# Optimization experiments

Hardware: AMD Instinct MI355X
Metric: run time of the kernel (lower is better)

Reference implementation:

```python
import jax, jax.numpy as jnp
import numpy as np

B, N, E, H = 4, 4096, 1024, 16
D = E // H


def setup_inputs() -> dict:
    key = jax.random.key(0)
    ks = jax.random.split(key, 8)
    s = 1.0 / np.sqrt(E)
    x = jax.random.normal(ks[0], (B, N, E), dtype=jnp.float32)
    # binary multiplicative sparsity pattern over the head-head score matrix
    sparsity_pattern = jax.random.randint(ks[1], (H, H), 0, 2).astype(jnp.float32)
    Wq = jax.random.normal(ks[2], (E, E), dtype=jnp.float32) * s
    bq = jax.random.normal(ks[3], (E,), dtype=jnp.float32) * s
    Wk = jax.random.normal(ks[4], (E, E), dtype=jnp.float32) * s
    bk = jax.random.normal(ks[5], (E,), dtype=jnp.float32) * s
    Wv = jax.random.normal(ks[6], (E, E), dtype=jnp.float32) * s
    bv = jax.random.normal(ks[7], (E,), dtype=jnp.float32) * s
    return {"x": x, "sparsity_pattern": sparsity_pattern,
            "Wq": Wq, "bq": bq, "Wk": Wk, "bk": bk, "Wv": Wv, "bv": bv}


def reference(x, sparsity_pattern, Wq, bq, Wk, bk, Wv, bv):
    b, n, e = x.shape
    # torch Linear: y = x @ W.T + b
    q = (x @ Wq.T + bq).reshape(b, n, H, D)
    k = (x @ Wk.T + bk).reshape(b, n, H, D)
    v = (x @ Wv.T + bv).reshape(b, n, H, D)
    # torch.matmul over last two dims of [B,N,H,D]: scores are [B,N,H,H]
    scores = jnp.einsum('bnhd,bngd->bnhg', q, k) * sparsity_pattern
    attn = jax.nn.softmax(scores, axis=-1)
    out = jnp.einsum('bnhg,bngd->bnhd', attn, v).reshape(b, n, e)
    return out
```

## Files before the change

### kernel.cpp

```cpp
#include <hip/hip_runtime.h>
#include <hip/hip_bf16.h>

#define M_   16384
#define K_   1024
#define NQKV 3072

typedef _Float16 f16x4 __attribute__((ext_vector_type(4)));
typedef _Float16 f16x8 __attribute__((ext_vector_type(8)));
typedef float    f32x4 __attribute__((ext_vector_type(4)));

__global__ __launch_bounds__(256) void cvt_f32_f16(const float* __restrict__ in,
                                                   _Float16* __restrict__ o, int n4) {
  int i = blockIdx.x * blockDim.x + threadIdx.x;
  const int stride = gridDim.x * blockDim.x;
  for (; i < n4; i += stride) {
    float4 v = ((const float4*)in)[i];
    f16x4 h; h[0] = (_Float16)v.x; h[1] = (_Float16)v.y;
    h[2] = (_Float16)v.z; h[3] = (_Float16)v.w;
    *(f16x4*)&o[(size_t)i * 4] = h;
  }
}

__global__ __launch_bounds__(256) void gemm_qkv(
    const _Float16* __restrict__ xh, const _Float16* __restrict__ wh,
    const float* __restrict__ bq, const float* __restrict__ bk,
    const float* __restrict__ bv, _Float16* __restrict__ qkv)
{
  __shared__ __align__(16) _Float16 As[128 * 64];
  __shared__ __align__(16) _Float16 Bs[128 * 64];

  const int tid  = threadIdx.x;
  const int ln   = tid & 63;
  const int w    = tid >> 6;
  const int wm   = w >> 1, wn = w & 1;
  const int lcol = ln & 15, quad = ln >> 4;

  const int m0 = blockIdx.y * 128;
  const int n0 = blockIdx.x * 128;

  f32x4 acc[4][4];
#pragma unroll
  for (int i = 0; i < 4; i++)
#pragma unroll
    for (int j = 0; j < 4; j++) acc[i][j] = f32x4{0.f, 0.f, 0.f, 0.f};

  for (int k0 = 0; k0 < K_; k0 += 64) {
#pragma unroll
    for (int i = 0; i < 4; ++i) {
      const int cb  = w * 256 + i * 64;
      const int c   = cb + ln;
      const int row = c >> 3, cc = c & 7;
      __builtin_amdgcn_global_load_lds(
          (const __attribute__((address_space(1))) void*)(xh + (size_t)(m0 + row) * K_ + k0 + cc * 8),
          (__attribute__((address_space(3))) void*)(As + (size_t)cb * 8), 16, 0, 0);
      __builtin_amdgcn_global_load_lds(
          (const __attribute__((address_space(1))) void*)(wh + (size_t)(n0 + row) * K_ + k0 + cc * 8),
          (__attribute__((address_space(3))) void*)(Bs + (size_t)cb * 8), 16, 0, 0);
    }
    __syncthreads();

#pragma unroll
    for (int kk = 0; kk < 64; kk += 32) {
      f16x8 a[4], b[4];
#pragma unroll
      for (int mi = 0; mi < 4; mi++)
        a[mi] = *(const f16x8*)&As[(wm * 64 + mi * 16 + lcol) * 64 + kk + quad * 8];
#pragma unroll
      for (int ni = 0; ni < 4; ni++)
        b[ni] = *(const f16x8*)&Bs[(wn * 64 + ni * 16 + lcol) * 64 + kk + quad * 8];
#pragma unroll
      for (int mi = 0; mi < 4; mi++)
#pragma unroll
        for (int ni = 0; ni < 4; ni++)
          acc[mi][ni] = __builtin_amdgcn_mfma_f32_16x16x32_f16(a[mi], b[ni], acc[mi][ni], 0, 0, 0);
    }
    __syncthreads();
  }

#pragma unroll
  for (int ni = 0; ni < 4; ni++) {
    const int col = n0 + wn * 64 + ni * 16 + lcol;
    const int seg = col >> 10, cs = col & 1023;
    const float bi = ((seg == 0) ? bq : (seg == 1) ? bk : bv)[cs];
#pragma unroll
    for (int mi = 0; mi < 4; mi++) {
      const int r0 = m0 + wm * 64 + mi * 16 + quad * 4;
#pragma unroll
      for (int r = 0; r < 4; r++)
        qkv[(size_t)(r0 + r) * 3072 + col] = (_Float16)(acc[mi][ni][r] + bi);
    }
  }
}

__global__ __launch_bounds__(256) void attn_kernel(
    const _Float16* __restrict__ qkv,
    const float* __restrict__ pat,
    float* __restrict__ out)
{
  __shared__ float pat_s[256];
  __shared__ __align__(16) _Float16 Ps[4][16 * 24];
  __shared__ __align__(16) _Float16 Vt[4][64 * 24];

  const int tid  = threadIdx.x;
  const int ln   = tid & 63;
  const int wv   = tid >> 6;
  const int lcol = ln & 15, quad = ln >> 4;
  const int t    = blockIdx.x * 4 + wv;

  pat_s[tid] = pat[tid];
  __syncthreads();

  const _Float16* qg = qkv + (size_t)t * 3072;
  const _Float16* kg = qg + 1024;
  const _Float16* vg = qg + 2048;

#pragma unroll
  for (int i = 0; i < 2; i++) {
    const int e = i * 64 + ln;
    const int g = e >> 3, c = (e & 7) * 8;
    f16x8 vc = *(const f16x8*)(vg + g * 64 + c);
#pragma unroll
    for (int j = 0; j < 8; j++) Vt[wv][(c + j) * 24 + g] = vc[j];
  }

  f16x8 aq0 = *(const f16x8*)(qg + lcol * 64 + quad * 8);
  f16x8 aq1 = *(const f16x8*)(qg + lcol * 64 + 32 + quad * 8);
  f16x8 bk0 = *(const f16x8*)(kg + lcol * 64 + quad * 8);
  f16x8 bk1 = *(const f16x8*)(kg + lcol * 64 + 32 + quad * 8);
  f32x4 s = {0.f, 0.f, 0.f, 0.f};
  s = __builtin_amdgcn_mfma_f32_16x16x32_f16(aq0, bk0, s, 0, 0, 0);
  s = __builtin_amdgcn_mfma_f32_16x16x32_f16(aq1, bk1, s, 0, 0, 0);

#pragma unroll
  for (int r = 0; r < 4; r++) {
    const float sv = s[r] * pat_s[(quad * 4 + r) * 16 + lcol];
    float m = sv;
#pragma unroll
    for (int msk = 1; msk < 16; msk <<= 1) m = fmaxf(m, __shfl_xor(m, msk, 64));
    const float e = __expf(sv - m);
    float su = e;
#pragma unroll
    for (int msk = 1; msk < 16; msk <<= 1) su += __shfl_xor(su, msk, 64);
    Ps[wv][(quad * 4 + r) * 24 + lcol] = (_Float16)(e / su);
  }

  f16x8 ap = {};
  if (quad < 2) ap = *(const f16x8*)&Ps[wv][lcol * 24 + quad * 8];

  f32x4 o[4];
#pragma unroll
  for (int dt = 0; dt < 4; dt++) {
    f16x8 bvf = {};
    if (quad < 2) bvf = *(const f16x8*)&Vt[wv][(dt * 16 + lcol) * 24 + quad * 8];
    f32x4 z = {0.f, 0.f, 0.f, 0.f};
    o[dt] = __builtin_amdgcn_mfma_f32_16x16x32_f16(ap, bvf, z, 0, 0, 0);
  }

  float* op = out + (size_t)t * 1024;
#pragma unroll
  for (int dt = 0; dt < 4; dt++)
#pragma unroll
    for (int r = 0; r < 4; r++)
      op[(quad * 4 + r) * 64 + dt * 16 + lcol] = o[dt][r];
}

extern "C" void kernel_launch(void* const* d_in, const int* in_sizes, int n_in,
                              void* d_out, int out_size, void* d_ws, size_t ws_size,
                              hipStream_t stream) {
  const float* x   = (const float*)d_in[0];
  const float* pat = (const float*)d_in[1];
  const float* Wq  = (const float*)d_in[2];
  const float* bq  = (const float*)d_in[3];
  const float* Wk  = (const float*)d_in[4];
  const float* bk  = (const float*)d_in[5];
  const float* Wv  = (const float*)d_in[6];
  const float* bv  = (const float*)d_in[7];

  _Float16* qkvh = (_Float16*)d_ws;
  _Float16* xh   = qkvh + (size_t)50331648;
  _Float16* wh   = qkvh + (size_t)67108864;

  cvt_f32_f16<<<4096, 256, 0, stream>>>(x,  xh,               4194304);
  cvt_f32_f16<<<1024, 256, 0, stream>>>(Wq, wh,                262144);
  cvt_f32_f16<<<1024, 256, 0, stream>>>(Wk, wh + 1048576,      262144);
  cvt_f32_f16<<<1024, 256, 0, stream>>>(Wv, wh + 2097152,      262144);

  dim3 g1(NQKV / 128, M_ / 128);
  gemm_qkv<<<g1, 256, 0, stream>>>(xh, wh, bq, bk, bv, qkvh);
  attn_kernel<<<M_ / 4, 256, 0, stream>>>(qkvh, pat, (float*)d_out);
}
```

Measured before the change: 313.9 us.

## Enlarge QKV GEMM tiles to 256x256 with double-buffered swizzled LDS pipeline

Rewrites the QKV projection GEMM to use 256x256 block tiles with 8 waves. It adds double-buffered LDS with prefetch of the next K slice, XOR-swizzled LDS layout to avoid bank conflicts, and interleaved sub-tile MFMA phases with priority hints. Blocks are remapped so neighbouring tiles land on the same XCD for L2 reuse. Larger tiles raise arithmetic intensity but use 128KB LDS and many accumulator registers, limiting occupancy to one block per CU.

```diff
diff --git a/kernel.cpp b/kernel.cpp
--- a/kernel.cpp
+++ b/kernel.cpp
@@ -21,75 +21,122 @@
   }
 }
 
-__global__ __launch_bounds__(256) void gemm_qkv(
+__global__ __launch_bounds__(512, 2) void gemm_qkv(
     const _Float16* __restrict__ xh, const _Float16* __restrict__ wh,
     const float* __restrict__ bq, const float* __restrict__ bk,
     const float* __restrict__ bv, _Float16* __restrict__ qkv)
 {
-  __shared__ __align__(16) _Float16 As[128 * 64];
-  __shared__ __align__(16) _Float16 Bs[128 * 64];
+  __shared__ __align__(16) _Float16 As[2][256 * 64];
+  __shared__ __align__(16) _Float16 Bs[2][256 * 64];
 
   const int tid  = threadIdx.x;
   const int ln   = tid & 63;
   const int w    = tid >> 6;
-  const int wm   = w >> 1, wn = w & 1;
+  const int wm2  = w >> 2;
+  const int wn4  = w & 3;
   const int lcol = ln & 15, quad = ln >> 4;
 
-  const int m0 = blockIdx.y * 128;
-  const int n0 = blockIdx.x * 128;
-
-  f32x4 acc[4][4];
-#pragma unroll
-  for (int i = 0; i < 4; i++)
-#pragma unroll
-    for (int j = 0; j < 4; j++) acc[i][j] = f32x4{0.f, 0.f, 0.f, 0.f};
-
-  for (int k0 = 0; k0 < K_; k0 += 64) {
-#pragma unroll
-    for (int i = 0; i < 4; ++i) {
-      const int cb  = w * 256 + i * 64;
-      const int c   = cb + ln;
-      const int row = c >> 3, cc = c & 7;
-      __builtin_amdgcn_global_load_lds(
-          (const __attribute__((address_space(1))) void*)(xh + (size_t)(m0 + row) * K_ + k0 + cc * 8),
-          (__attribute__((address_space(3))) void*)(As + (size_t)cb * 8), 16, 0, 0);
-      __builtin_amdgcn_global_load_lds(
-          (const __attribute__((address_space(1))) void*)(wh + (size_t)(n0 + row) * K_ + k0 + cc * 8),
-          (__attribute__((address_space(3))) void*)(Bs + (size_t)cb * 8), 16, 0, 0);
-    }
-    __syncthreads();
-
-#pragma unroll
-    for (int kk = 0; kk < 64; kk += 32) {
-      f16x8 a[4], b[4];
-#pragma unroll
-      for (int mi = 0; mi < 4; mi++)
-        a[mi] = *(const f16x8*)&As[(wm * 64 + mi * 16 + lcol) * 64 + kk + quad * 8];
-#pragma unroll
-      for (int ni = 0; ni < 4; ni++)
-        b[ni] = *(const f16x8*)&Bs[(wn * 64 + ni * 16 + lcol) * 64 + kk + quad * 8];
-#pragma unroll
-      for (int mi = 0; mi < 4; mi++)
-#pragma unroll
-        for (int ni = 0; ni < 4; ni++)
-          acc[mi][ni] = __builtin_amdgcn_mfma_f32_16x16x32_f16(a[mi], b[ni], acc[mi][ni], 0, 0, 0);
-    }
-    __syncthreads();
-  }
-
-#pragma unroll
-  for (int ni = 0; ni < 4; ni++) {
-    const int col = n0 + wn * 64 + ni * 16 + lcol;
+  const int bid = blockIdx.x;
+  const int swz = (bid & 7) * 96 + (bid >> 3);
+  const int m0 = (swz / 12) * 256;
+  const int n0 = (swz % 12) * 256;
+
+  f32x4 acc[8][4];
+#pragma unroll
+  for (int i = 0; i < 8; ++i)
+#pragma unroll
+    for (int j = 0; j < 4; ++j) acc[i][j] = f32x4{0.f, 0.f, 0.f, 0.f};
+
+#define STAGE(BUF, T)                                                          \
+  {                                                                            \
+    const int k0s = (T) * 64;                                                  \
+    _Pragma("unroll")                                                          \
+    for (int i = 0; i < 4; ++i) {                                              \
+      const int c  = i * 512 + tid;                                            \
+      const int r  = c >> 3;                                                   \
+      const int cb = (c & 7) ^ (r & 7);                                        \
+      const int db = (i * 512 + w * 64) * 8;       \
+      __builtin_amdgcn_global_load_lds(                                        \
+          (const __attribute__((address_space(1))) void*)(                     \
+              xh + (size_t)(m0 + r) * K_ + k0s + cb * 8),                      \
+          (__attribute__((address_space(3))) void*)(&As[BUF][db]), 16, 0, 0);  \
+      __builtin_amdgcn_global_load_lds(                                        \
+          (const __attribute__((address_space(1))) void*)(                     \
+              wh + (size_t)(n0 + r) * K_ + k0s + cb * 8),                      \
+          (__attribute__((address_space(3))) void*)(&Bs[BUF][db]), 16, 0, 0);  \
+    }                                                                          \
+  }
+
+  f16x8 a[4][2], b[2][2];
+
+#define LOADA(MH)                                                              \
+  _Pragma("unroll")                                                            \
+  for (int mi = 0; mi < 4; ++mi) {                                             \
+    const int ar = wm2 * 128 + (MH) * 64 + mi * 16 + lcol;                     \
+    const int sw = ar & 7;                                                     \
+    a[mi][0] = *(const f16x8*)&As[cur][ar * 64 + ((quad    ) ^ sw) * 8];       \
+    a[mi][1] = *(const f16x8*)&As[cur][ar * 64 + ((quad + 4) ^ sw) * 8];       \
+  }
+
+#define LOADB(NH)                                                              \
+  _Pragma("unroll")                                                            \
+  for (int ni = 0; ni < 2; ++ni) {                                             \
+    const int br = wn4 * 64 + (NH) * 32 + ni * 16 + lcol;                      \
+    const int sw = br & 7;                                                     \
+    b[ni][0] = *(const f16x8*)&Bs[cur][br * 64 + ((quad    ) ^ sw) * 8];       \
+    b[ni][1] = *(const f16x8*)&Bs[cur][br * 64 + ((quad + 4) ^ sw) * 8];       \
+  }
+
+#define MFMA16(MH, NH)                                                         \
+  __builtin_amdgcn_s_setprio(1);                                               \
+  _Pragma("unroll")                                                            \
+  for (int kb = 0; kb < 2; ++kb)                                               \
+    _Pragma("unroll")                                                          \
+    for (int mi = 0; mi < 4; ++mi)                                             \
+      _Pragma("unroll")                                                        \
+      for (int ni = 0; ni < 2; ++ni)                                           \
+        acc[(MH) * 4 + mi][(NH) * 2 + ni] =                                    \
+            __builtin_amdgcn_mfma_f32_16x16x32_f16(                            \
+                a[mi][kb], b[ni][kb], acc[(MH) * 4 + mi][(NH) * 2 + ni],       \
+                0, 0, 0);                                                      \
+  __builtin_amdgcn_s_setprio(0);
+
+  STAGE(0, 0);
+  asm volatile("s_waitcnt vmcnt(0)" ::: "memory");
+  __builtin_amdgcn_s_barrier();
+
+  for (int t = 0; t < 16; ++t) {
+    const int cur = t & 1;
+    if (t < 15) STAGE(cur ^ 1, t + 1);
+
+    LOADA(0); LOADB(0); MFMA16(0, 0);
+    __builtin_amdgcn_s_barrier(); __builtin_amdgcn_sched_barrier(0);
+    LOADA(1);           MFMA16(1, 0);
+    __builtin_amdgcn_s_barrier(); __builtin_amdgcn_sched_barrier(0);
+              LOADB(1); MFMA16(1, 1);
+    __builtin_amdgcn_s_barrier(); __builtin_amdgcn_sched_barrier(0);
+    LOADA(0);           MFMA16(0, 1);
+    if (t < 15) asm volatile("s_waitcnt vmcnt(0)" ::: "memory");
+    __builtin_amdgcn_s_barrier(); __builtin_amdgcn_sched_barrier(0);
+  }
+
+#pragma unroll
+  for (int nh = 0; nh < 4; ++nh) {
+    const int col = n0 + wn4 * 64 + nh * 16 + lcol;
     const int seg = col >> 10, cs = col & 1023;
     const float bi = ((seg == 0) ? bq : (seg == 1) ? bk : bv)[cs];
 #pragma unroll
-    for (int mi = 0; mi < 4; mi++) {
-      const int r0 = m0 + wm * 64 + mi * 16 + quad * 4;
-#pragma unroll
-      for (int r = 0; r < 4; r++)
-        qkv[(size_t)(r0 + r) * 3072 + col] = (_Float16)(acc[mi][ni][r] + bi);
+    for (int mi = 0; mi < 8; ++mi) {
+      const int r0 = m0 + wm2 * 128 + mi * 16 + quad * 4;
+#pragma unroll
+      for (int r = 0; r < 4; ++r)
+        qkv[(size_t)(r0 + r) * 3072 + col] = (_Float16)(acc[mi][nh][r] + bi);
     }
   }
+#undef STAGE
+#undef LOADA
+#undef LOADB
+#undef MFMA16
 }
 
 __global__ __launch_bounds__(256) void attn_kernel(
@@ -185,7 +232,6 @@
   cvt_f32_f16<<<1024, 256, 0, stream>>>(Wk, wh + 1048576,      262144);
   cvt_f32_f16<<<1024, 256, 0, stream>>>(Wv, wh + 2097152,      262144);
 
-  dim3 g1(NQKV / 128, M_ / 128);
-  gemm_qkv<<<g1, 256, 0, stream>>>(xh, wh, bq, bk, bv, qkvh);
+  gemm_qkv<<<768, 512, 0, stream>>>(xh, wh, bq, bk, bv, qkvh);
   attn_kernel<<<M_ / 4, 256, 0, stream>>>(qkvh, pat, (float*)d_out);
 }
```

After: 292.3 us. 1.07x faster.
